# Optimization experiments

Hardware: AMD Instinct MI355X
Metric: run time of the kernel (lower is better)

The kernel has to match this reference:

```python
import jax, jax.numpy as jnp
import numpy as np
from jax import lax

BN_EPS = 1e-5


def setup_inputs() -> dict:
    key = jax.random.key(0)
    k = jax.random.split(key, 7)
    B, H, W = 128, 224, 224
    return {
        "x": jax.random.normal(k[0], (B, 1, H, W), dtype=jnp.float32),
        "conv_w": jax.random.normal(k[1], (16, 1, 5, 5), dtype=jnp.float32) * 0.1,
        "conv_b": jax.random.normal(k[2], (16,), dtype=jnp.float32) * 0.1,
        "gamma": jax.random.uniform(k[3], (16,), dtype=jnp.float32, minval=0.5, maxval=1.5),
        "beta": jax.random.normal(k[4], (16,), dtype=jnp.float32) * 0.1,
        "run_mean": jax.random.normal(k[5], (16,), dtype=jnp.float32) * 0.1,
        "run_var": jax.random.uniform(k[6], (16,), dtype=jnp.float32, minval=0.5, maxval=1.5),
    }


def reference(x, conv_w, conv_b, gamma, beta, run_mean, run_var):
    # Conv2d(1,16,5,stride=1,padding=2): NCHW x OIHW -> NCHW
    y = lax.conv_general_dilated(
        x, conv_w, window_strides=(1, 1), padding=[(2, 2), (2, 2)],
        dimension_numbers=("NCHW", "OIHW", "NCHW"))
    y = y + conv_b[None, :, None, None]
    # BatchNorm2d(16) in inference form with running stats
    scale = gamma * lax.rsqrt(run_var + BN_EPS)
    y = y * scale[None, :, None, None] + (beta - run_mean * scale)[None, :, None, None]
    # ReLU
    y = jnp.maximum(y, 0.0)
    # MaxPool2d(kernel=2, stride=2)
    out = lax.reduce_window(y, -jnp.inf, lax.max,
                            window_dimensions=(1, 1, 2, 2),
                            window_strides=(1, 1, 2, 2),
                            padding="VALID")
    return out  # [B, 16, H/2, W/2]
```

## Files before the change

kernel.cpp:

```cpp
#include <hip/hip_runtime.h>
#include <stdint.h>

#define TILE_P 16
#define TILE_C 32
#define HALO 2
#define IN_TILE 36
#define IMG 224
#define OUT_DIM 112
#define NCH 16
#define PAIR_STRIDE 40

typedef __fp16 half2_t __attribute__((ext_vector_type(2)));

#define WS_WPAIRS 32

__global__ void prep_kernel(const float* __restrict__ conv_w,
                            const float* __restrict__ conv_b,
                            const float* __restrict__ gamma,
                            const float* __restrict__ beta,
                            const float* __restrict__ run_mean,
                            const float* __restrict__ run_var,
                            uint32_t* __restrict__ ws)
{
    int ch = threadIdx.x;
    if (ch >= NCH) return;
    float s = gamma[ch] * rsqrtf(run_var[ch] + 1e-5f);
    float t = fmaf(s, conv_b[ch] - run_mean[ch], beta[ch]);
    float2* st = (float2*)ws;
    st[ch] = make_float2(s, t);

    uint32_t* wp = ws + WS_WPAIRS + ch * 20;
    const float* w = conv_w + ch * 25;
    for (int r = 0; r < 5; ++r) {
        half2_t A = __builtin_amdgcn_cvt_pkrtz(w[r*5+0], w[r*5+1]);
        half2_t B = __builtin_amdgcn_cvt_pkrtz(w[r*5+2], w[r*5+3]);
        half2_t C = __builtin_amdgcn_cvt_pkrtz(w[r*5+4], 0.f);
        half2_t D = __builtin_amdgcn_cvt_pkrtz(0.f, w[r*5+4]);
        wp[r*4+0] = __builtin_bit_cast(uint32_t, A);
        wp[r*4+1] = __builtin_bit_cast(uint32_t, B);
        wp[r*4+2] = __builtin_bit_cast(uint32_t, C);
        wp[r*4+3] = __builtin_bit_cast(uint32_t, D);
    }
}

__device__ __forceinline__ half2_t ld_pair(const uint32_t* p) {
    return __builtin_bit_cast(half2_t, *p);
}

__global__ __launch_bounds__(256)
void conv_bn_relu_pool(const float* __restrict__ x,
                       const uint32_t* __restrict__ ws,
                       float* __restrict__ out)
{
    __shared__ float T[IN_TILE * IN_TILE];
    __shared__ uint32_t P[IN_TILE * PAIR_STRIDE];

    const int tid = threadIdx.x;
    const int b  = blockIdx.z;
    const int ty = blockIdx.y * TILE_C;
    const int tx = blockIdx.x * TILE_C;

    const float* xb = x + (size_t)b * IMG * IMG;

    for (int i = tid; i < IN_TILE * IN_TILE; i += 256) {
        int r = i / IN_TILE, c = i - r * IN_TILE;
        int gy = ty - HALO + r, gx = tx - HALO + c;
        float v = 0.f;
        if ((unsigned)gy < IMG && (unsigned)gx < IMG) v = xb[gy * IMG + gx];
        T[i] = v;
    }
    __syncthreads();

    for (int i = tid; i < IN_TILE * (IN_TILE - 1); i += 256) {
        int r = i / (IN_TILE - 1), c = i - r * (IN_TILE - 1);
        half2_t h = __builtin_amdgcn_cvt_pkrtz(T[r * IN_TILE + c], T[r * IN_TILE + c + 1]);
        P[r * PAIR_STRIDE + c] = __builtin_bit_cast(uint32_t, h);
    }
    __syncthreads();

    const int px = tid & 15;
    const int py = tid >> 4;
    const uint32_t* prow = P + (2 * py) * PAIR_STRIDE + 2 * px;

    const int oy = blockIdx.y * TILE_P + py;
    const int ox = blockIdx.x * TILE_P + px;
    float* outb = out + (size_t)b * NCH * (OUT_DIM * OUT_DIM) + oy * OUT_DIM + ox;

    const float2* st = (const float2*)ws;

    #pragma unroll 1
    for (int g = 0; g < 4; ++g) {
        const uint32_t* wp = ws + WS_WPAIRS + g * 80;
        float acc[4][4];
        #pragma unroll
        for (int i = 0; i < 4; ++i)
            #pragma unroll
            for (int j = 0; j < 4; ++j) acc[i][j] = 0.f;

        #pragma unroll
        for (int r = 0; r < 5; ++r) {
            const uint32_t* p0 = prow + r * PAIR_STRIDE;
            const uint32_t* p1 = p0 + PAIR_STRIDE;
            half2_t q00 = ld_pair(p0 + 0), q01 = ld_pair(p0 + 1);
            half2_t q02 = ld_pair(p0 + 2), q03 = ld_pair(p0 + 3);
            half2_t q04 = ld_pair(p0 + 4);
            half2_t q10 = ld_pair(p1 + 0), q11 = ld_pair(p1 + 1);
            half2_t q12 = ld_pair(p1 + 2), q13 = ld_pair(p1 + 3);
            half2_t q14 = ld_pair(p1 + 4);
            #pragma unroll
            for (int i = 0; i < 4; ++i) {
                half2_t A = __builtin_bit_cast(half2_t, wp[i*20 + r*4 + 0]);
                half2_t B = __builtin_bit_cast(half2_t, wp[i*20 + r*4 + 1]);
                half2_t C = __builtin_bit_cast(half2_t, wp[i*20 + r*4 + 2]);
                half2_t D = __builtin_bit_cast(half2_t, wp[i*20 + r*4 + 3]);
                acc[i][0] = __builtin_amdgcn_fdot2(q00, A,
                            __builtin_amdgcn_fdot2(q02, B,
                            __builtin_amdgcn_fdot2(q04, C, acc[i][0], false), false), false);
                acc[i][1] = __builtin_amdgcn_fdot2(q01, A,
                            __builtin_amdgcn_fdot2(q03, B,
                            __builtin_amdgcn_fdot2(q04, D, acc[i][1], false), false), false);
                acc[i][2] = __builtin_amdgcn_fdot2(q10, A,
                            __builtin_amdgcn_fdot2(q12, B,
                            __builtin_amdgcn_fdot2(q14, C, acc[i][2], false), false), false);
                acc[i][3] = __builtin_amdgcn_fdot2(q11, A,
                            __builtin_amdgcn_fdot2(q13, B,
                            __builtin_amdgcn_fdot2(q14, D, acc[i][3], false), false), false);
            }
        }

        #pragma unroll
        for (int i = 0; i < 4; ++i) {
            int ch = g * 4 + i;
            float m = fmaxf(fmaxf(acc[i][0], acc[i][1]), fmaxf(acc[i][2], acc[i][3]));
            float2 s_t = st[ch];
            float y = fmaxf(fmaf(m, s_t.x, s_t.y), 0.f);
            outb[ch * (OUT_DIM * OUT_DIM)] = y;
        }
    }
}

extern "C" void kernel_launch(void* const* d_in, const int* in_sizes, int n_in,
                              void* d_out, int out_size, void* d_ws, size_t ws_size,
                              hipStream_t stream) {
    const float* x        = (const float*)d_in[0];
    const float* conv_w   = (const float*)d_in[1];
    const float* conv_b   = (const float*)d_in[2];
    const float* gamma    = (const float*)d_in[3];
    const float* beta     = (const float*)d_in[4];
    const float* run_mean = (const float*)d_in[5];
    const float* run_var  = (const float*)d_in[6];
    float* out = (float*)d_out;
    uint32_t* ws = (uint32_t*)d_ws;

    prep_kernel<<<1, 64, 0, stream>>>(conv_w, conv_b, gamma, beta, run_mean, run_var, ws);

    dim3 grid(IMG / TILE_C, IMG / TILE_C, 128);
    dim3 block(256);
    conv_bn_relu_pool<<<grid, block, 0, stream>>>(x, ws, out);
}
```

Measured before the change: 173.5 us.

## Compute 5x5 conv with MFMA f16 16x16x32 instead of packed fdot2

Recasts the 16-channel 5x5 convolution as matrix-core MFMA products: the 25 weights plus padding form a 32-wide K dimension held in a per-lane B fragment, and input pixel pairs are gathered from shared memory as the A fragment. The staging step is merged into a single pass that converts floats straight to packed half pairs, dropping one shared buffer and one barrier. Each wave handles output rows and writes float2 results. This relies on a non-obvious K-index mapping between weights and gathered pixels, and the output stores become strided per channel.

```diff
diff --git a/kernel.cpp b/kernel.cpp
--- a/kernel.cpp
+++ b/kernel.cpp
@@ -1,18 +1,19 @@
 #include <hip/hip_runtime.h>
 #include <stdint.h>
 
-#define TILE_P 16
-#define TILE_C 32
-#define HALO 2
-#define IN_TILE 36
 #define IMG 224
 #define OUT_DIM 112
 #define NCH 16
-#define PAIR_STRIDE 40
+#define TILE 32
+#define P_ROWS 36
+#define P_COLS 36
+#define P_STRIDE 48
 
-typedef __fp16 half2_t __attribute__((ext_vector_type(2)));
+typedef _Float16 h8t  __attribute__((ext_vector_type(8)));
+typedef float    f32x4 __attribute__((ext_vector_type(4)));
+typedef uint32_t u32x4 __attribute__((ext_vector_type(4)));
 
-#define WS_WPAIRS 32
+#define WS_B1 32
 
 __global__ void prep_kernel(const float* __restrict__ conv_w,
                             const float* __restrict__ conv_b,
@@ -22,29 +23,31 @@
                             const float* __restrict__ run_var,
                             uint32_t* __restrict__ ws)
 {
-    int ch = threadIdx.x;
-    if (ch >= NCH) return;
-    float s = gamma[ch] * rsqrtf(run_var[ch] + 1e-5f);
-    float t = fmaf(s, conv_b[ch] - run_mean[ch], beta[ch]);
-    float2* st = (float2*)ws;
-    st[ch] = make_float2(s, t);
+    int l = threadIdx.x;
+    if (l >= 64) return;
+    if (l < NCH) {
+        float s = gamma[l] * rsqrtf(run_var[l] + 1e-5f);
+        float t = fmaf(s, conv_b[l] - run_mean[l], beta[l]);
+        ((float2*)ws)[l] = make_float2(s, t);
+    }
+    const int ch = l & 15;
+    const int g  = l >> 4;
+    const float* w = conv_w + ch * 25;
 
-    uint32_t* wp = ws + WS_WPAIRS + ch * 20;
-    const float* w = conv_w + ch * 25;
-    for (int r = 0; r < 5; ++r) {
-        half2_t A = __builtin_amdgcn_cvt_pkrtz(w[r*5+0], w[r*5+1]);
-        half2_t B = __builtin_amdgcn_cvt_pkrtz(w[r*5+2], w[r*5+3]);
-        half2_t C = __builtin_amdgcn_cvt_pkrtz(w[r*5+4], 0.f);
-        half2_t D = __builtin_amdgcn_cvt_pkrtz(0.f, w[r*5+4]);
-        wp[r*4+0] = __builtin_bit_cast(uint32_t, A);
-        wp[r*4+1] = __builtin_bit_cast(uint32_t, B);
-        wp[r*4+2] = __builtin_bit_cast(uint32_t, C);
-        wp[r*4+3] = __builtin_bit_cast(uint32_t, D);
-    }
-}
+    float w0 = w[g * 5 + 0], w1 = w[g * 5 + 1], w2 = w[g * 5 + 2];
+    float w3 = w[g * 5 + 3], w4 = w[g * 5 + 4];
+    const float* wr4 = w + 20;
+    float e0 = (2 * g + 0 < 5) ? wr4[2 * g + 0] : 0.f;
+    float e1 = (2 * g + 1 < 5) ? wr4[2 * g + 1] : 0.f;
 
-__device__ __forceinline__ half2_t ld_pair(const uint32_t* p) {
-    return __builtin_bit_cast(half2_t, *p);
+    auto p0 = __builtin_amdgcn_cvt_pkrtz(w0, w1);
+    auto p1 = __builtin_amdgcn_cvt_pkrtz(w2, w3);
+    auto p2 = __builtin_amdgcn_cvt_pkrtz(w4, 0.f);
+    auto p3 = __builtin_amdgcn_cvt_pkrtz(e0, e1);
+    ws[WS_B1 + l * 4 + 0] = __builtin_bit_cast(uint32_t, p0);
+    ws[WS_B1 + l * 4 + 1] = __builtin_bit_cast(uint32_t, p1);
+    ws[WS_B1 + l * 4 + 2] = __builtin_bit_cast(uint32_t, p2);
+    ws[WS_B1 + l * 4 + 3] = __builtin_bit_cast(uint32_t, p3);
 }
 
 __global__ __launch_bounds__(256)
@@ -52,89 +55,67 @@
                        const uint32_t* __restrict__ ws,
                        float* __restrict__ out)
 {
-    __shared__ float T[IN_TILE * IN_TILE];
-    __shared__ uint32_t P[IN_TILE * PAIR_STRIDE];
+    __shared__ uint32_t P[P_ROWS * P_STRIDE];
 
     const int tid = threadIdx.x;
     const int b  = blockIdx.z;
-    const int ty = blockIdx.y * TILE_C;
-    const int tx = blockIdx.x * TILE_C;
-
+    const int ty = blockIdx.y * TILE;
+    const int tx = blockIdx.x * TILE;
     const float* xb = x + (size_t)b * IMG * IMG;
 
-    for (int i = tid; i < IN_TILE * IN_TILE; i += 256) {
-        int r = i / IN_TILE, c = i - r * IN_TILE;
-        int gy = ty - HALO + r, gx = tx - HALO + c;
-        float v = 0.f;
-        if ((unsigned)gy < IMG && (unsigned)gx < IMG) v = xb[gy * IMG + gx];
-        T[i] = v;
+    for (int i = tid; i < P_ROWS * P_STRIDE; i += 256) {
+        int r = i / P_STRIDE, c = i - r * P_STRIDE;
+        float v0 = 0.f, v1 = 0.f;
+        int gy = ty - 2 + r;
+        int gx = tx - 2 + c;
+        if (c < P_COLS && (unsigned)gy < IMG) {
+            const float* row = xb + gy * IMG;
+            if ((unsigned)gx < IMG) v0 = row[gx];
+            if ((unsigned)(gx + 1) < IMG) v1 = row[gx + 1];
+        }
+        auto p = __builtin_amdgcn_cvt_pkrtz(v0, v1);
+        P[i] = __builtin_bit_cast(uint32_t, p);
     }
+
+    const int lane = tid & 63;
+    const int wv   = tid >> 6;
+    const int pp   = lane & 15;
+    const int g    = lane >> 4;
+
+    u32x4 b1u = *(const u32x4*)(ws + WS_B1 + lane * 4);
+    h8t  B1 = __builtin_bit_cast(h8t, b1u);
+    float2 sst = ((const float2*)ws)[pp];
+
     __syncthreads();
 
-    for (int i = tid; i < IN_TILE * (IN_TILE - 1); i += 256) {
-        int r = i / (IN_TILE - 1), c = i - r * (IN_TILE - 1);
-        half2_t h = __builtin_amdgcn_cvt_pkrtz(T[r * IN_TILE + c], T[r * IN_TILE + c + 1]);
-        P[r * PAIR_STRIDE + c] = __builtin_bit_cast(uint32_t, h);
-    }
-    __syncthreads();
+    float* outb = out + ((size_t)b * NCH + pp) * (OUT_DIM * OUT_DIM);
 
-    const int px = tid & 15;
-    const int py = tid >> 4;
-    const uint32_t* prow = P + (2 * py) * PAIR_STRIDE + 2 * px;
+    for (int s = 0; s < 4; ++s) {
+        const int yl = 8 * wv + 2 * s;
+        const int oy = (ty >> 1) + 4 * wv + s;
+        #pragma unroll
+        for (int sub = 0; sub < 2; ++sub) {
+            const int cb = sub * 16 + pp;
+            const uint32_t* rA = P + (yl + g) * P_STRIDE + cb;
+            const uint32_t* r4 = P + (yl + 4) * P_STRIDE + cb + 2*g;
 
-    const int oy = blockIdx.y * TILE_P + py;
-    const int ox = blockIdx.x * TILE_P + px;
-    float* outb = out + (size_t)b * NCH * (OUT_DIM * OUT_DIM) + oy * OUT_DIM + ox;
+            f32x4 accA = {0.f, 0.f, 0.f, 0.f};
+            f32x4 accB = {0.f, 0.f, 0.f, 0.f};
 
-    const float2* st = (const float2*)ws;
+            u32x4 a1 = {rA[0], rA[2], rA[4], r4[0]};
+            accA = __builtin_amdgcn_mfma_f32_16x16x32_f16(
+                       __builtin_bit_cast(h8t, a1), B1, accA, 0, 0, 0);
+            u32x4 c1 = {rA[P_STRIDE], rA[P_STRIDE + 2], rA[P_STRIDE + 4], r4[P_STRIDE]};
+            accB = __builtin_amdgcn_mfma_f32_16x16x32_f16(
+                       __builtin_bit_cast(h8t, c1), B1, accB, 0, 0, 0);
 
-    #pragma unroll 1
-    for (int g = 0; g < 4; ++g) {
-        const uint32_t* wp = ws + WS_WPAIRS + g * 80;
-        float acc[4][4];
-        #pragma unroll
-        for (int i = 0; i < 4; ++i)
-            #pragma unroll
-            for (int j = 0; j < 4; ++j) acc[i][j] = 0.f;
+            float m0 = fmaxf(fmaxf(accA[0], accA[1]), fmaxf(accB[0], accB[1]));
+            float m1 = fmaxf(fmaxf(accA[2], accA[3]), fmaxf(accB[2], accB[3]));
+            float y0 = fmaxf(fmaf(m0, sst.x, sst.y), 0.f);
+            float y1 = fmaxf(fmaf(m1, sst.x, sst.y), 0.f);
 
-        #pragma unroll
-        for (int r = 0; r < 5; ++r) {
-            const uint32_t* p0 = prow + r * PAIR_STRIDE;
-            const uint32_t* p1 = p0 + PAIR_STRIDE;
-            half2_t q00 = ld_pair(p0 + 0), q01 = ld_pair(p0 + 1);
-            half2_t q02 = ld_pair(p0 + 2), q03 = ld_pair(p0 + 3);
-            half2_t q04 = ld_pair(p0 + 4);
-            half2_t q10 = ld_pair(p1 + 0), q11 = ld_pair(p1 + 1);
-            half2_t q12 = ld_pair(p1 + 2), q13 = ld_pair(p1 + 3);
-            half2_t q14 = ld_pair(p1 + 4);
-            #pragma unroll
-            for (int i = 0; i < 4; ++i) {
-                half2_t A = __builtin_bit_cast(half2_t, wp[i*20 + r*4 + 0]);
-                half2_t B = __builtin_bit_cast(half2_t, wp[i*20 + r*4 + 1]);
-                half2_t C = __builtin_bit_cast(half2_t, wp[i*20 + r*4 + 2]);
-                half2_t D = __builtin_bit_cast(half2_t, wp[i*20 + r*4 + 3]);
-                acc[i][0] = __builtin_amdgcn_fdot2(q00, A,
-                            __builtin_amdgcn_fdot2(q02, B,
-                            __builtin_amdgcn_fdot2(q04, C, acc[i][0], false), false), false);
-                acc[i][1] = __builtin_amdgcn_fdot2(q01, A,
-                            __builtin_amdgcn_fdot2(q03, B,
-                            __builtin_amdgcn_fdot2(q04, D, acc[i][1], false), false), false);
-                acc[i][2] = __builtin_amdgcn_fdot2(q10, A,
-                            __builtin_amdgcn_fdot2(q12, B,
-                            __builtin_amdgcn_fdot2(q14, C, acc[i][2], false), false), false);
-                acc[i][3] = __builtin_amdgcn_fdot2(q11, A,
-                            __builtin_amdgcn_fdot2(q13, B,
-                            __builtin_amdgcn_fdot2(q14, D, acc[i][3], false), false), false);
-            }
-        }
-
-        #pragma unroll
-        for (int i = 0; i < 4; ++i) {
-            int ch = g * 4 + i;
-            float m = fmaxf(fmaxf(acc[i][0], acc[i][1]), fmaxf(acc[i][2], acc[i][3]));
-            float2 s_t = st[ch];
-            float y = fmaxf(fmaf(m, s_t.x, s_t.y), 0.f);
-            outb[ch * (OUT_DIM * OUT_DIM)] = y;
+            const int ox = (tx >> 1) + sub * 8 + 2 * g;
+            *(float2*)(outb + oy * OUT_DIM + ox) = make_float2(y0, y1);
         }
     }
 }
@@ -154,7 +135,7 @@
 
     prep_kernel<<<1, 64, 0, stream>>>(conv_w, conv_b, gamma, beta, run_mean, run_var, ws);
 
-    dim3 grid(IMG / TILE_C, IMG / TILE_C, 128);
+    dim3 grid(IMG / TILE, IMG / TILE, 128);
     dim3 block(256);
     conv_bn_relu_pool<<<grid, block, 0, stream>>>(x, ws, out);
 }
```

After: 172.2 us. No clear change (-0.8%).
